# Kernel optimization log

Measured on AMD Instinct MI355X. Metric: run time of the kernel, lower is better.

Reference implementation:

```python
import jax, jax.numpy as jnp
import numpy as np

N_NODES = 100000
N_EDGES = 1600000
NFEAT, NHID, NCLASS = 256, 128, 64


def gcn_conv(x, edge_index, edge_weight, W):
    # PyG GCNConv (normalize=False, add_self_loops=False, bias=False):
    # h = x @ W.T; out[i] = sum over edges (j->i) of w_e * h[j]
    h = x @ W.T                                   # [N, out]
    src, dst = edge_index[0], edge_index[1]
    msgs = h[src] * edge_weight[:, None]          # [E, out]
    return jax.ops.segment_sum(msgs, dst, num_segments=x.shape[0])


def setup_inputs() -> dict:
    key = jax.random.key(0)
    ks = jax.random.split(key, 7)
    x = jax.random.normal(ks[0], (N_NODES, NFEAT), dtype=jnp.float32)
    edge_index1 = jax.random.randint(ks[1], (2, N_EDGES), 0, N_NODES, dtype=jnp.int64)
    edge_index2 = jax.random.randint(ks[2], (2, N_EDGES), 0, N_NODES, dtype=jnp.int64)
    edge_weight1 = jax.random.uniform(ks[3], (N_EDGES,), dtype=jnp.float32)
    edge_weight2 = jax.random.uniform(ks[4], (N_EDGES,), dtype=jnp.float32)
    W1 = jax.random.normal(ks[5], (NHID, NFEAT), dtype=jnp.float32) * (1.0 / np.sqrt(NFEAT))
    W2 = jax.random.normal(ks[6], (NCLASS, NHID), dtype=jnp.float32) * (1.0 / np.sqrt(NHID))
    return {"x": x, "edge_index1": edge_index1, "edge_index2": edge_index2,
            "edge_weight1": edge_weight1, "edge_weight2": edge_weight2,
            "W1": W1, "W2": W2}


def reference(x, edge_index1, edge_index2, edge_weight1, edge_weight2, W1, W2):
    h = jax.nn.relu(gcn_conv(x, edge_index1, edge_weight1, W1))
    out = gcn_conv(h, edge_index2, edge_weight2, W2)
    return out
```

## Files before the change

kernel.cpp:

```cpp
#include <hip/hip_runtime.h>

typedef __attribute__((ext_vector_type(8))) short short8;
typedef __attribute__((ext_vector_type(4))) float floatx4;

#define BKT_SHIFT 8
#define BKT_MASK 255
#define CAP 5120

__device__ __forceinline__ ushort f2bf(float f) {
    uint u = __builtin_bit_cast(uint, f);
    uint r = (u + 0x7FFFu + ((u >> 16) & 1u)) >> 16;
    return (ushort)r;
}
__device__ __forceinline__ float bf2f(ushort u) {
    return __builtin_bit_cast(float, (uint)u << 16);
}
__device__ __forceinline__ float bflo(uint h) {
    return __builtin_bit_cast(float, h << 16);
}
__device__ __forceinline__ float bfhi(uint h) {
    return __builtin_bit_cast(float, h & 0xffff0000u);
}

__global__ __launch_bounds__(256) void prep(const uint* __restrict__ ei,
                                            int* __restrict__ flag,
                                            const float* __restrict__ W1,
                                            const float* __restrict__ W2,
                                            ushort* __restrict__ w1b,
                                            ushort* __restrict__ w2b, int n1, int n2) {
    if (blockIdx.x == 0 && threadIdx.x < 64) {
        uint v = ei[2 * threadIdx.x + 1];
        unsigned long long b = __ballot(v != 0u);
        if (threadIdx.x == 0) *flag = (b == 0ull) ? 1 : 0;
    }
    int i = blockIdx.x * 256 + threadIdx.x;
    if (i < n1) w1b[i] = f2bf(W1[i]);
    else if (i < n1 + n2) w2b[i - n1] = f2bf(W2[i - n1]);
}

__global__ __launch_bounds__(256) void cvt_x(const float* __restrict__ X,
                                             ushort* __restrict__ XB, long n) {
    long i = ((long)blockIdx.x * 256 + threadIdx.x) * 8;
    if (i < n) {
        floatx4 a = *(const floatx4*)(X + i);
        floatx4 b = *(const floatx4*)(X + i + 4);
        short8 o;
        #pragma unroll
        for (int j = 0; j < 4; j++) {
            o[j]     = (short)f2bf(a[j]);
            o[4 + j] = (short)f2bf(b[j]);
        }
        *(short8*)(XB + i) = o;
    }
}

template<int K, int NOUT>
__global__ __launch_bounds__(256) void gemm_bt(const ushort* __restrict__ Xb,
                                               const ushort* __restrict__ W,
                                               ushort* __restrict__ Y, int N) {
    constexpr int NT = NOUT / 16;
    constexpr int KS = K / 32;
    constexpr int ROWS = 64;
    constexpr int RB = K * 2;
    constexpr int LPR = RB / 16;
    constexpr int RPI = 64 / LPR;
    constexpr int NI = 16 / RPI;
    __shared__ __align__(16) char xs[ROWS * RB];

    const int tid  = threadIdx.x;
    const int lane = tid & 63;
    const int wv   = tid >> 6;
    const int t    = lane & 15;
    const int q    = lane >> 4;
    const int rbase = blockIdx.x * ROWS;

    #pragma unroll
    for (int i = 0; i < NI; i++) {
        int rl0 = wv * 16 + i * RPI;
        int grow0 = rbase + rl0;
        if (grow0 < N) {
            int rl = rl0 + lane / LPR;
            const char* src = (const char*)Xb + (long)grow0 * RB + (lane / LPR) * RB
                            + (((lane % LPR) * 16) ^ ((rl & 7) << 5));
            __builtin_amdgcn_global_load_lds(
                (const __attribute__((address_space(1))) void*)src,
                (__attribute__((address_space(3))) void*)&xs[rl0 * RB], 16, 0, 0);
        }
    }
    __syncthreads();

    floatx4 acc[NT];
    #pragma unroll
    for (int b = 0; b < NT; b++)
        #pragma unroll
        for (int i = 0; i < 4; i++) acc[b][i] = 0.f;

    const int lrow = wv * 16 + t;
    const char* xrow = &xs[lrow * RB];
    const uint swz = (uint)((t & 7) << 5);

    for (int ks = 0; ks < KS; ks++) {
        short8 af = *(const short8*)(xrow + (((uint)(ks * 64 + q * 16)) ^ swz));
        #pragma unroll
        for (int nt = 0; nt < NT; nt++) {
            short8 bf = *(const short8*)(W + (long)(nt * 16 + t) * K + ks * 32 + q * 8);
            acc[nt] = __builtin_amdgcn_mfma_f32_16x16x32_bf16(af, bf, acc[nt], 0, 0, 0);
        }
    }

    const int obase = rbase + wv * 16;
    #pragma unroll
    for (int j = 0; j < 4; j++) {
        int orow = obase + q * 4 + j;
        if (orow < N) {
            #pragma unroll
            for (int nt = 0; nt < NT; nt++)
                Y[(long)orow * NOUT + nt * 16 + t] = f2bf(acc[nt][j]);
        }
    }
}

__global__ __launch_bounds__(256) void bin_edges(const void* __restrict__ eidx,
                                                 const float* __restrict__ ew,
                                                 int* __restrict__ cntg,
                                                 int2* __restrict__ binA, int E, int nbk,
                                                 const int* __restrict__ flag) {
    __shared__ int lc[512], lb[512], lo[512];
    for (int t = threadIdx.x; t < 512; t += 256) { lc[t] = 0; lo[t] = 0; }
    __syncthreads();
    int S = (E + gridDim.x - 1) / gridDim.x;
    int s = blockIdx.x * S, e = min(E, s + S);
    bool f = *flag;
    for (int i = s + threadIdx.x; i < e; i += 256) {
        int dst = f ? (int)((const long long*)eidx)[i + E] : ((const int*)eidx)[i + E];
        atomicAdd(&lc[dst >> BKT_SHIFT], 1);
    }
    __syncthreads();
    for (int t = threadIdx.x; t < nbk; t += 256)
        lb[t] = lc[t] ? atomicAdd(&cntg[t], lc[t]) : 0;
    __syncthreads();
    for (int i = s + threadIdx.x; i < e; i += 256) {
        int src, dst;
        if (f) { const long long* p = (const long long*)eidx; src = (int)p[i]; dst = (int)p[i + E]; }
        else   { const int* p = (const int*)eidx;             src = p[i];      dst = p[i + E]; }
        int bk = dst >> BKT_SHIFT;
        int pos = lb[bk] + atomicAdd(&lo[bk], 1);
        if (pos < CAP)
            binA[(long)bk * CAP + pos] = make_int2(src | ((dst & BKT_MASK) << 24),
                                                   __builtin_bit_cast(int, ew[i]));
    }
}

__global__ __launch_bounds__(256) void sort_bucket(const int2* __restrict__ binA,
                                                   const int* __restrict__ cntg,
                                                   int2* __restrict__ pairs,
                                                   int2* __restrict__ rr, int N) {
    __shared__ int hcnt[256], hcur[256];
    __shared__ int2 ps[CAP];
    int b = blockIdx.x, t = threadIdx.x;
    const long base = (long)b * CAP;
    int n = min(cntg[b], CAP);
    hcnt[t] = 0; hcur[t] = 0;
    __syncthreads();
    for (int i = t; i < n; i += 256)
        atomicAdd(&hcnt[(uint)binA[base + i].x >> 24], 1);
    __syncthreads();
    for (int off = 1; off < 256; off <<= 1) {
        int v = (t >= off) ? hcnt[t - off] : 0;
        __syncthreads();
        hcnt[t] += v;
        __syncthreads();
    }
    int node = (b << BKT_SHIFT) + t;
    int ex = t ? hcnt[t - 1] : 0;
    if (node < N) rr[node] = make_int2((int)base + ex, (int)base + hcnt[t]);
    __syncthreads();
    for (int i = t; i < n; i += 256) {
        int2 p = binA[base + i];
        int dl = (uint)p.x >> 24;
        int pos = (dl ? hcnt[dl - 1] : 0) + atomicAdd(&hcur[dl], 1);
        ps[pos] = make_int2(p.x & 0x00FFFFFF, p.y);
    }
    __syncthreads();
    for (int j = t; j < n; j += 256) pairs[base + j] = ps[j];
}

template<int F, bool RELU, bool BF16OUT>
__global__ __launch_bounds__(256) void gather_nodes(const ushort* __restrict__ H,
                                                    const int2* __restrict__ pairs,
                                                    const int2* __restrict__ rr,
                                                    void* __restrict__ out, int N) {
    constexpr int L = F / 2;
    constexpr int NPW = 64 / L;
    int wave = (blockIdx.x * 256 + threadIdx.x) >> 6;
    int lane = threadIdx.x & 63;
    int node = wave * NPW + lane / L;
    int c = lane % L;
    if (node >= N) return;
    int2 se = rr[node];
    int s = se.x, e = se.y;
    float a0 = 0.f, a1 = 0.f, b0 = 0.f, b1 = 0.f;
    float c0 = 0.f, c1 = 0.f, d0 = 0.f, d1 = 0.f;
    int i = s;
    int e8 = s + ((e - s) & ~7);
    for (; i < e8; i += 8) {
        int2 p0 = pairs[i],     p1 = pairs[i + 1], p2 = pairs[i + 2], p3 = pairs[i + 3];
        int2 p4 = pairs[i + 4], p5 = pairs[i + 5], p6 = pairs[i + 6], p7 = pairs[i + 7];
        uint h0 = *(const uint*)(H + (long)p0.x * F + 2 * c);
        uint h1 = *(const uint*)(H + (long)p1.x * F + 2 * c);
        uint h2 = *(const uint*)(H + (long)p2.x * F + 2 * c);
        uint h3 = *(const uint*)(H + (long)p3.x * F + 2 * c);
        uint h4 = *(const uint*)(H + (long)p4.x * F + 2 * c);
        uint h5 = *(const uint*)(H + (long)p5.x * F + 2 * c);
        uint h6 = *(const uint*)(H + (long)p6.x * F + 2 * c);
        uint h7 = *(const uint*)(H + (long)p7.x * F + 2 * c);
        float w0 = __builtin_bit_cast(float, p0.y), w1 = __builtin_bit_cast(float, p1.y);
        float w2 = __builtin_bit_cast(float, p2.y), w3 = __builtin_bit_cast(float, p3.y);
        float w4 = __builtin_bit_cast(float, p4.y), w5 = __builtin_bit_cast(float, p5.y);
        float w6 = __builtin_bit_cast(float, p6.y), w7 = __builtin_bit_cast(float, p7.y);
        a0 += w0 * bflo(h0);  a1 += w0 * bfhi(h0);
        b0 += w1 * bflo(h1);  b1 += w1 * bfhi(h1);
        c0 += w2 * bflo(h2);  c1 += w2 * bfhi(h2);
        d0 += w3 * bflo(h3);  d1 += w3 * bfhi(h3);
        a0 += w4 * bflo(h4);  a1 += w4 * bfhi(h4);
        b0 += w5 * bflo(h5);  b1 += w5 * bfhi(h5);
        c0 += w6 * bflo(h6);  c1 += w6 * bfhi(h6);
        d0 += w7 * bflo(h7);  d1 += w7 * bfhi(h7);
    }
    for (; i < e; i++) {
        int2 p = pairs[i];
        uint h = *(const uint*)(H + (long)p.x * F + 2 * c);
        float w = __builtin_bit_cast(float, p.y);
        a0 += w * bflo(h);  a1 += w * bfhi(h);
    }
    float r0 = (a0 + b0) + (c0 + d0);
    float r1 = (a1 + b1) + (c1 + d1);
    if (BF16OUT) {
        if (RELU) { r0 = fmaxf(r0, 0.f); r1 = fmaxf(r1, 0.f); }
        uint packed = (uint)f2bf(r0) | ((uint)f2bf(r1) << 16);
        ((uint*)out)[(long)node * L + c] = packed;
    } else {
        float2 r; r.x = r0; r.y = r1;
        ((float2*)out)[(long)node * L + c] = r;
    }
}

extern "C" void kernel_launch(void* const* d_in, const int* in_sizes, int n_in,
                              void* d_out, int out_size, void* d_ws, size_t ws_size,
                              hipStream_t stream) {
    const float* x   = (const float*)d_in[0];
    const void*  ei1 = d_in[1];
    const void*  ei2 = d_in[2];
    const float* ew1 = (const float*)d_in[3];
    const float* ew2 = (const float*)d_in[4];
    const float* W1  = (const float*)d_in[5];
    const float* W2  = (const float*)d_in[6];

    const int N = in_sizes[0] / 256;
    const int E = in_sizes[3];
    const int NBK = (N + 255) >> 8;

    char* ws = (char*)d_ws;
    size_t off = 0;
    ushort* XW     = (ushort*)(ws + off); off += (size_t)N * 128 * 2;
    ushort* hbuf   = (ushort*)(ws + off); off += (size_t)N * 128 * 2;
    int2*   binA   = (int2*)  (ws + off); off += (size_t)NBK * CAP * 8;
    int2*   pairs  = (int2*)  (ws + off); off += (size_t)NBK * CAP * 8;
    int2*   rr     = (int2*)  (ws + off); off += (size_t)N * 8;
    int*    cnt    = (int*)   (ws + off); off += 512 * 4;
    ushort* w1b    = (ushort*)(ws + off); off += 128 * 256 * 2;
    ushort* w2b    = (ushort*)(ws + off); off += 64 * 128 * 2;
    int*    flag   = (int*)   (ws + off);
    ushort* XB     = hbuf;
    ushort* H2     = XW;

    prep<<<160, 256, 0, stream>>>((const uint*)ei1, flag, W1, W2, w1b, w2b,
                                  128 * 256, 64 * 128);
    cvt_x<<<(int)(((long)N * 256 / 8 + 255) / 256), 256, 0, stream>>>(x, XB, (long)N * 256);

    int gblocks = (N + 63) / 64;
    gemm_bt<256, 128><<<gblocks, 256, 0, stream>>>(XB, w1b, XW, N);

    hipMemsetAsync(cnt, 0, 512 * 4, stream);
    bin_edges<<<256, 256, 0, stream>>>(ei1, ew1, cnt, binA, E, NBK, flag);
    sort_bucket<<<NBK, 256, 0, stream>>>(binA, cnt, pairs, rr, N);
    gather_nodes<128, true, true><<<(N + 3) / 4, 256, 0, stream>>>(
        XW, pairs, rr, hbuf, N);

    gemm_bt<128, 64><<<gblocks, 256, 0, stream>>>(hbuf, w2b, H2, N);
    hipMemsetAsync(cnt, 0, 512 * 4, stream);
    bin_edges<<<256, 256, 0, stream>>>(ei2, ew2, cnt, binA, E, NBK, flag);
    sort_bucket<<<NBK, 256, 0, stream>>>(binA, cnt, pairs, rr, N);
    gather_nodes<64, false, false><<<(N * 2 + 7) / 8, 256, 0, stream>>>(
        H2, pairs, rr, (float*)d_out, N);
}
```

Measured before the change: 511.1 us.

## Use one wave per node with edge-parallel lane groups; shrink buckets; drop memsets

The gather kernel now gives each node a whole wave. Lanes split into groups that handle different edges, each lane loads 8-byte vectors of features, and partial sums are combined with xor shuffles. This targets load imbalance and the per-lane serial edge loop of the old one-node-per-partial-wave layout. Buckets shrink from 256 to 128 nodes, which means more sort blocks with less shared memory each. The two memset calls are replaced by zeroing both counter arrays inside prep. Risks are more shuffle work, and CAP overflow on buckets that are denser than expected.

```diff
diff --git a/kernel.cpp b/kernel.cpp
--- a/kernel.cpp
+++ b/kernel.cpp
@@ -3,17 +3,14 @@
 typedef __attribute__((ext_vector_type(8))) short short8;
 typedef __attribute__((ext_vector_type(4))) float floatx4;
 
-#define BKT_SHIFT 8
-#define BKT_MASK 255
-#define CAP 5120
+#define BKT_SHIFT 7
+#define BKT_MASK 127
+#define CAP 2560
 
 __device__ __forceinline__ ushort f2bf(float f) {
     uint u = __builtin_bit_cast(uint, f);
     uint r = (u + 0x7FFFu + ((u >> 16) & 1u)) >> 16;
     return (ushort)r;
-}
-__device__ __forceinline__ float bf2f(ushort u) {
-    return __builtin_bit_cast(float, (uint)u << 16);
 }
 __device__ __forceinline__ float bflo(uint h) {
     return __builtin_bit_cast(float, h << 16);
@@ -27,13 +24,16 @@
                                             const float* __restrict__ W1,
                                             const float* __restrict__ W2,
                                             ushort* __restrict__ w1b,
-                                            ushort* __restrict__ w2b, int n1, int n2) {
+                                            ushort* __restrict__ w2b,
+                                            int* __restrict__ cntz,
+                                            int n1, int n2) {
     if (blockIdx.x == 0 && threadIdx.x < 64) {
         uint v = ei[2 * threadIdx.x + 1];
         unsigned long long b = __ballot(v != 0u);
         if (threadIdx.x == 0) *flag = (b == 0ull) ? 1 : 0;
     }
     int i = blockIdx.x * 256 + threadIdx.x;
+    if (i < 2048) cntz[i] = 0;
     if (i < n1) w1b[i] = f2bf(W1[i]);
     else if (i < n1 + n2) w2b[i - n1] = f2bf(W2[i - n1]);
 }
@@ -125,8 +125,8 @@
                                                  int* __restrict__ cntg,
                                                  int2* __restrict__ binA, int E, int nbk,
                                                  const int* __restrict__ flag) {
-    __shared__ int lc[512], lb[512], lo[512];
-    for (int t = threadIdx.x; t < 512; t += 256) { lc[t] = 0; lo[t] = 0; }
+    __shared__ int lc[1024], lb[1024], lo[1024];
+    for (int t = threadIdx.x; t < 1024; t += 256) { lc[t] = 0; lo[t] = 0; }
     __syncthreads();
     int S = (E + gridDim.x - 1) / gridDim.x;
     int s = blockIdx.x * S, e = min(E, s + S);
@@ -155,25 +155,27 @@
                                                    const int* __restrict__ cntg,
                                                    int2* __restrict__ pairs,
                                                    int2* __restrict__ rr, int N) {
-    __shared__ int hcnt[256], hcur[256];
+    __shared__ int hcnt[128], hcur[128];
     __shared__ int2 ps[CAP];
     int b = blockIdx.x, t = threadIdx.x;
     const long base = (long)b * CAP;
     int n = min(cntg[b], CAP);
-    hcnt[t] = 0; hcur[t] = 0;
+    if (t < 128) { hcnt[t] = 0; hcur[t] = 0; }
     __syncthreads();
     for (int i = t; i < n; i += 256)
         atomicAdd(&hcnt[(uint)binA[base + i].x >> 24], 1);
     __syncthreads();
-    for (int off = 1; off < 256; off <<= 1) {
-        int v = (t >= off) ? hcnt[t - off] : 0;
+    for (int off = 1; off < 128; off <<= 1) {
+        int v = (t >= off && t < 128) ? hcnt[t - off] : 0;
         __syncthreads();
-        hcnt[t] += v;
+        if (t < 128) hcnt[t] += v;
         __syncthreads();
     }
-    int node = (b << BKT_SHIFT) + t;
-    int ex = t ? hcnt[t - 1] : 0;
-    if (node < N) rr[node] = make_int2((int)base + ex, (int)base + hcnt[t]);
+    if (t < 128) {
+        int node = (b << BKT_SHIFT) + t;
+        int ex = t ? hcnt[t - 1] : 0;
+        if (node < N) rr[node] = make_int2((int)base + ex, (int)base + hcnt[t]);
+    }
     __syncthreads();
     for (int i = t; i < n; i += 256) {
         int2 p = binA[base + i];
@@ -190,58 +192,78 @@
                                                     const int2* __restrict__ pairs,
                                                     const int2* __restrict__ rr,
                                                     void* __restrict__ out, int N) {
-    constexpr int L = F / 2;
-    constexpr int NPW = 64 / L;
+    constexpr int LPE = F / 4;
+    constexpr int G   = 64 / LPE;
+    constexpr int U   = 4;
     int wave = (blockIdx.x * 256 + threadIdx.x) >> 6;
     int lane = threadIdx.x & 63;
-    int node = wave * NPW + lane / L;
-    int c = lane % L;
+    int node = wave;
     if (node >= N) return;
+    const int g  = lane / LPE;
+    const int cL = lane % LPE;
     int2 se = rr[node];
     int s = se.x, e = se.y;
-    float a0 = 0.f, a1 = 0.f, b0 = 0.f, b1 = 0.f;
-    float c0 = 0.f, c1 = 0.f, d0 = 0.f, d1 = 0.f;
-    int i = s;
-    int e8 = s + ((e - s) & ~7);
-    for (; i < e8; i += 8) {
-        int2 p0 = pairs[i],     p1 = pairs[i + 1], p2 = pairs[i + 2], p3 = pairs[i + 3];
-        int2 p4 = pairs[i + 4], p5 = pairs[i + 5], p6 = pairs[i + 6], p7 = pairs[i + 7];
-        uint h0 = *(const uint*)(H + (long)p0.x * F + 2 * c);
-        uint h1 = *(const uint*)(H + (long)p1.x * F + 2 * c);
-        uint h2 = *(const uint*)(H + (long)p2.x * F + 2 * c);
-        uint h3 = *(const uint*)(H + (long)p3.x * F + 2 * c);
-        uint h4 = *(const uint*)(H + (long)p4.x * F + 2 * c);
-        uint h5 = *(const uint*)(H + (long)p5.x * F + 2 * c);
-        uint h6 = *(const uint*)(H + (long)p6.x * F + 2 * c);
-        uint h7 = *(const uint*)(H + (long)p7.x * F + 2 * c);
+
+    float a0 = 0.f, a1 = 0.f, a2 = 0.f, a3 = 0.f;
+    float b0 = 0.f, b1 = 0.f, b2 = 0.f, b3 = 0.f;
+    float c0 = 0.f, c1 = 0.f, c2 = 0.f, c3 = 0.f;
+    float d0 = 0.f, d1 = 0.f, d2 = 0.f, d3 = 0.f;
+
+    int cnt = e - s;
+    int full = cnt / (G * U);
+    for (int k = 0; k < full; k++) {
+        int idx = s + k * U * G + g;
+        int2 p0 = pairs[idx];
+        int2 p1 = pairs[idx + G];
+        int2 p2 = pairs[idx + 2 * G];
+        int2 p3 = pairs[idx + 3 * G];
+        uint2 h0 = *(const uint2*)(H + (long)p0.x * F + 4 * cL);
+        uint2 h1 = *(const uint2*)(H + (long)p1.x * F + 4 * cL);
+        uint2 h2 = *(const uint2*)(H + (long)p2.x * F + 4 * cL);
+        uint2 h3 = *(const uint2*)(H + (long)p3.x * F + 4 * cL);
         float w0 = __builtin_bit_cast(float, p0.y), w1 = __builtin_bit_cast(float, p1.y);
         float w2 = __builtin_bit_cast(float, p2.y), w3 = __builtin_bit_cast(float, p3.y);
-        float w4 = __builtin_bit_cast(float, p4.y), w5 = __builtin_bit_cast(float, p5.y);
-        float w6 = __builtin_bit_cast(float, p6.y), w7 = __builtin_bit_cast(float, p7.y);
-        a0 += w0 * bflo(h0);  a1 += w0 * bfhi(h0);
-        b0 += w1 * bflo(h1);  b1 += w1 * bfhi(h1);
-        c0 += w2 * bflo(h2);  c1 += w2 * bfhi(h2);
-        d0 += w3 * bflo(h3);  d1 += w3 * bfhi(h3);
-        a0 += w4 * bflo(h4);  a1 += w4 * bfhi(h4);
-        b0 += w5 * bflo(h5);  b1 += w5 * bfhi(h5);
-        c0 += w6 * bflo(h6);  c1 += w6 * bfhi(h6);
-        d0 += w7 * bflo(h7);  d1 += w7 * bfhi(h7);
-    }
-    for (; i < e; i++) {
-        int2 p = pairs[i];
-        uint h = *(const uint*)(H + (long)p.x * F + 2 * c);
+        a0 += w0 * bflo(h0.x);  a1 += w0 * bfhi(h0.x);
+        a2 += w0 * bflo(h0.y);  a3 += w0 * bfhi(h0.y);
+        b0 += w1 * bflo(h1.x);  b1 += w1 * bfhi(h1.x);
+        b2 += w1 * bflo(h1.y);  b3 += w1 * bfhi(h1.y);
+        c0 += w2 * bflo(h2.x);  c1 += w2 * bfhi(h2.x);
+        c2 += w2 * bflo(h2.y);  c3 += w2 * bfhi(h2.y);
+        d0 += w3 * bflo(h3.x);  d1 += w3 * bfhi(h3.x);
+        d2 += w3 * bflo(h3.y);  d3 += w3 * bfhi(h3.y);
+    }
+    for (int idx = s + full * U * G + g; idx < e; idx += G) {
+        int2 p = pairs[idx];
+        uint2 h = *(const uint2*)(H + (long)p.x * F + 4 * cL);
         float w = __builtin_bit_cast(float, p.y);
-        a0 += w * bflo(h);  a1 += w * bfhi(h);
+        a0 += w * bflo(h.x);  a1 += w * bfhi(h.x);
+        a2 += w * bflo(h.y);  a3 += w * bfhi(h.y);
     }
     float r0 = (a0 + b0) + (c0 + d0);
     float r1 = (a1 + b1) + (c1 + d1);
-    if (BF16OUT) {
-        if (RELU) { r0 = fmaxf(r0, 0.f); r1 = fmaxf(r1, 0.f); }
-        uint packed = (uint)f2bf(r0) | ((uint)f2bf(r1) << 16);
-        ((uint*)out)[(long)node * L + c] = packed;
-    } else {
-        float2 r; r.x = r0; r.y = r1;
-        ((float2*)out)[(long)node * L + c] = r;
+    float r2 = (a2 + b2) + (c2 + d2);
+    float r3 = (a3 + b3) + (c3 + d3);
+    #pragma unroll
+    for (int m = LPE; m < 64; m <<= 1) {
+        r0 += __shfl_xor(r0, m);
+        r1 += __shfl_xor(r1, m);
+        r2 += __shfl_xor(r2, m);
+        r3 += __shfl_xor(r3, m);
+    }
+    if (g == 0) {
+        if (BF16OUT) {
+            if (RELU) {
+                r0 = fmaxf(r0, 0.f); r1 = fmaxf(r1, 0.f);
+                r2 = fmaxf(r2, 0.f); r3 = fmaxf(r3, 0.f);
+            }
+            uint2 pk;
+            pk.x = (uint)f2bf(r0) | ((uint)f2bf(r1) << 16);
+            pk.y = (uint)f2bf(r2) | ((uint)f2bf(r3) << 16);
+            *(uint2*)((uint*)out + (long)node * (F / 2) + 2 * cL) = pk;
+        } else {
+            float4 r; r.x = r0; r.y = r1; r.z = r2; r.w = r3;
+            *(float4*)((float*)out + (long)node * F + 4 * cL) = r;
+        }
     }
 }
 
@@ -258,7 +280,7 @@
 
     const int N = in_sizes[0] / 256;
     const int E = in_sizes[3];
-    const int NBK = (N + 255) >> 8;
+    const int NBK = (N + BKT_MASK) >> BKT_SHIFT;
 
     char* ws = (char*)d_ws;
     size_t off = 0;
@@ -267,7 +289,8 @@
     int2*   binA   = (int2*)  (ws + off); off += (size_t)NBK * CAP * 8;
     int2*   pairs  = (int2*)  (ws + off); off += (size_t)NBK * CAP * 8;
     int2*   rr     = (int2*)  (ws + off); off += (size_t)N * 8;
-    int*    cnt    = (int*)   (ws + off); off += 512 * 4;
+    int*    cnt1   = (int*)   (ws + off); off += 1024 * 4;
+    int*    cnt2   = (int*)   (ws + off); off += 1024 * 4;
     ushort* w1b    = (ushort*)(ws + off); off += 128 * 256 * 2;
     ushort* w2b    = (ushort*)(ws + off); off += 64 * 128 * 2;
     int*    flag   = (int*)   (ws + off);
@@ -275,22 +298,20 @@
     ushort* H2     = XW;
 
     prep<<<160, 256, 0, stream>>>((const uint*)ei1, flag, W1, W2, w1b, w2b,
-                                  128 * 256, 64 * 128);
+                                  cnt1, 128 * 256, 64 * 128);
     cvt_x<<<(int)(((long)N * 256 / 8 + 255) / 256), 256, 0, stream>>>(x, XB, (long)N * 256);
 
     int gblocks = (N + 63) / 64;
     gemm_bt<256, 128><<<gblocks, 256, 0, stream>>>(XB, w1b, XW, N);
 
-    hipMemsetAsync(cnt, 0, 512 * 4, stream);
-    bin_edges<<<256, 256, 0, stream>>>(ei1, ew1, cnt, binA, E, NBK, flag);
-    sort_bucket<<<NBK, 256, 0, stream>>>(binA, cnt, pairs, rr, N);
+    bin_edges<<<256, 256, 0, stream>>>(ei1, ew1, cnt1, binA, E, NBK, flag);
+    sort_bucket<<<NBK, 256, 0, stream>>>(binA, cnt1, pairs, rr, N);
     gather_nodes<128, true, true><<<(N + 3) / 4, 256, 0, stream>>>(
         XW, pairs, rr, hbuf, N);
 
     gemm_bt<128, 64><<<gblocks, 256, 0, stream>>>(hbuf, w2b, H2, N);
-    hipMemsetAsync(cnt, 0, 512 * 4, stream);
-    bin_edges<<<256, 256, 0, stream>>>(ei2, ew2, cnt, binA, E, NBK, flag);
-    sort_bucket<<<NBK, 256, 0, stream>>>(binA, cnt, pairs, rr, N);
-    gather_nodes<64, false, false><<<(N * 2 + 7) / 8, 256, 0, stream>>>(
+    bin_edges<<<256, 256, 0, stream>>>(ei2, ew2, cnt2, binA, E, NBK, flag);
+    sort_bucket<<<NBK, 256, 0, stream>>>(binA, cnt2, pairs, rr, N);
+    gather_nodes<64, false, false><<<(N + 3) / 4, 256, 0, stream>>>(
         H2, pairs, rr, (float*)d_out, N);
 }
```

Measured after the change: 507.0 us. Within noise of the previous version (-0.8%).
